# Kernel tuning notes

Hardware: AMD Instinct MI355X
Metric: run time of the kernel (lower is better)

The kernel has to match this reference:

```python
import jax, jax.numpy as jnp
import numpy as np


def setup_inputs() -> dict:
    key = jax.random.key(0)
    k1, k2 = jax.random.split(key)
    B, C, H, W = 8, 128, 48, 48
    x = jax.random.normal(k1, (B, C, H, W), dtype=jnp.float32)
    y = jax.random.normal(k2, (B, C, H, W), dtype=jnp.float32)
    return {"x": x, "y": y}


def reference(x, y):
    # Pairwise squared-distance cost volume.
    # Original computes full Gram matrices xx, yy only for their diagonals;
    # here we compute the squared norms directly (same math, O(N*C) instead of O(N^2*C)).
    B, C, H, W = x.shape
    N = H * W
    xf = x.reshape(B, C, N)  # [B, C, N]
    yf = y.reshape(B, C, N)
    sx = jnp.sum(xf * xf, axis=1)  # [B, N], ||x_i||^2 (diag of x^T x)
    sy = jnp.sum(yf * yf, axis=1)  # [B, N], ||y_j||^2 (diag of y^T y)
    zz = jnp.einsum('bci,bcj->bij', yf, xf)  # zz[b,i,j] = y_i . x_j
    # P[b,i,j] = ||x_i||^2 + ||y_j||^2 - 2 * y_i . x_j  (matches rx^T + ry - 2*zz)
    P = sx[:, :, None] + sy[:, None, :] - 2.0 * zz
    return P.reshape(B, W * H, H, W)
```

## Files before the change

### kernel.cpp

```cpp
#include <hip/hip_runtime.h>

#define NTOK 2304
#define CC   128

typedef __attribute__((ext_vector_type(8))) short bf16x8;
typedef __attribute__((ext_vector_type(4))) float f32x4;

__device__ __forceinline__ unsigned f2bf(float f) {
  unsigned u = __builtin_bit_cast(unsigned, f);
  u += 0x7FFFu + ((u >> 16) & 1u);
  return (u >> 16) & 0xFFFFu;
}
__device__ __forceinline__ unsigned pk2(float a, float b) {
  return f2bf(a) | (f2bf(b) << 16);
}

__device__ __forceinline__ void g2l16(const void* g, void* l) {
  __builtin_amdgcn_global_load_lds(
      (const __attribute__((address_space(1))) unsigned int*)g,
      (__attribute__((address_space(3))) unsigned int*)l, 16, 0, 0);
}

__global__ __launch_bounds__(256) void pwd_prep(
    const float* __restrict__ x, const float* __restrict__ y,
    char* __restrict__ imgX, char* __restrict__ imgY,
    float* __restrict__ sx, float* __restrict__ sy) {
  __shared__ float part[8][32];
  const int tid = threadIdx.x;
  const int nl  = tid & 31;
  const int cg  = tid >> 5;
  const int n   = blockIdx.x * 32 + nl;
  const int b   = blockIdx.y;
  const int sel = blockIdx.z;
  const float* src = sel ? y : x;
  char* img = sel ? imgY : imgX;

  const float* p = src + ((size_t)b * CC + cg * 16) * NTOK + n;
  float v[16];
#pragma unroll
  for (int k = 0; k < 16; ++k) v[k] = p[(size_t)k * NTOK];

  float s = 0.f;
#pragma unroll
  for (int k = 0; k < 16; ++k) s = fmaf(v[k], v[k], s);
  part[cg][nl] = s;

  char* row = img + ((size_t)b * NTOK + n) * 256;
  const int swz = (n & 15) ^ ((n >> 4) & 3);
#pragma unroll
  for (int oo = 0; oo < 2; ++oo) {
    const int o = cg * 2 + oo;
    uint4 wv;
    wv.x = pk2(v[oo * 8 + 0], v[oo * 8 + 1]);
    wv.y = pk2(v[oo * 8 + 2], v[oo * 8 + 3]);
    wv.z = pk2(v[oo * 8 + 4], v[oo * 8 + 5]);
    wv.w = pk2(v[oo * 8 + 6], v[oo * 8 + 7]);
    *(uint4*)(row + ((o ^ swz) * 16)) = wv;
  }
  __syncthreads();
  if (tid < 32) {
    float t = 0.f;
#pragma unroll
    for (int g = 0; g < 8; ++g) t += part[g][tid];
    (sel ? sy : sx)[b * NTOK + blockIdx.x * 32 + tid] = t;
  }
}

__global__ __launch_bounds__(256, 5) void pwd_gemm(
    const char* __restrict__ imgX, const char* __restrict__ imgY,
    const float* __restrict__ sx, const float* __restrict__ sy,
    float* __restrict__ out) {
  __shared__ __attribute__((aligned(16))) char smem[32768];
  char* const smX = smem;
  char* const smY = smem + 16384;

  const int tid = threadIdx.x;

  const int bid = blockIdx.x;
  const int b   = bid & 7;
  const int rem = bid >> 3;
  const int byy = rem / 36;
  const int bxx = rem - byy * 36;
  const int i0 = byy * 64;
  const int j0 = bxx * 64;

  const int w  = tid >> 6;
  const int l  = tid & 63;
  const int lr = l & 15;
  const int lg = l >> 4;
  const int wi = w * 16;

  {
    const char* gx = imgX + ((size_t)b * NTOK + j0) * 256;
    const char* gy = imgY + ((size_t)b * NTOK + i0) * 256;
    const int wb = w * 4096;
    const size_t o0 = (size_t)wb + (size_t)l * 16;
#pragma unroll
    for (int it = 0; it < 4; ++it)
      g2l16(gx + o0 + it * 1024, smX + wb + it * 1024);
#pragma unroll
    for (int it = 0; it < 4; ++it)
      g2l16(gy + o0 + it * 1024, smY + wb + it * 1024);
  }

  const float sxr = sx[b * NTOK + i0 + wi + lr];
  f32x4 syq[4];
#pragma unroll
  for (int mf = 0; mf < 4; ++mf)
    syq[mf] = *(const f32x4*)(sy + b * NTOK + j0 + mf * 16 + lg * 4);

  __syncthreads();

  f32x4 acc[4] = {};
#pragma unroll
  for (int ks = 0; ks < 4; ++ks) {
    const int o = ks * 4 + lg;
    bf16x8 ax[4], by;
#pragma unroll
    for (int mf = 0; mf < 4; ++mf) {
      const int n = mf * 16 + lr;
      const int slot = o ^ (n & 15) ^ ((n >> 4) & 3);
      ax[mf] = *(const bf16x8*)(smX + n * 256 + slot * 16);
    }
    {
      const int n = wi + lr;
      const int slot = o ^ (n & 15) ^ ((n >> 4) & 3);
      by = *(const bf16x8*)(smY + n * 256 + slot * 16);
    }
#pragma unroll
    for (int mf = 0; mf < 4; ++mf)
      acc[mf] = __builtin_amdgcn_mfma_f32_16x16x32_bf16(ax[mf], by, acc[mf],
                                                        0, 0, 0);
  }

  {
    float* const tile = (float*)smem;
    __syncthreads();
#pragma unroll
    for (int mf = 0; mf < 4; ++mf) {
      f32x4 vv;
#pragma unroll
      for (int r = 0; r < 4; ++r)
        vv[r] = sxr + syq[mf][r] - 2.0f * acc[mf][r];
      const int row = wi + lr;
      const int c16 = mf * 4 + lg;
      *(f32x4*)((char*)tile + row * 256 + ((c16 ^ (row & 15)) * 16)) = vv;
    }
    __syncthreads();
#pragma unroll
    for (int it = 0; it < 4; ++it) {
      const int c   = it * 256 + tid;
      const int row = c >> 4;
      const int c16 = c & 15;
      f32x4 vv = *(const f32x4*)((char*)tile + row * 256 +
                                 ((c16 ^ (row & 15)) * 16));
      __builtin_nontemporal_store(
          vv, (f32x4*)(out + ((size_t)b * NTOK + i0 + row) * NTOK + j0 + c16 * 4));
    }
  }
}

extern "C" void kernel_launch(void* const* d_in, const int* in_sizes, int n_in,
                              void* d_out, int out_size, void* d_ws, size_t ws_size,
                              hipStream_t stream) {
  (void)in_sizes; (void)n_in; (void)out_size; (void)ws_size;
  const float* x = (const float*)d_in[0];
  const float* y = (const float*)d_in[1];
  float* out = (float*)d_out;

  char* imgX = (char*)d_ws;
  char* imgY = imgX + (size_t)8 * NTOK * 256;
  float* sx  = (float*)(imgY + (size_t)8 * NTOK * 256);
  float* sy  = sx + 8 * NTOK;

  dim3 gp(NTOK / 32, 8, 2);
  pwd_prep<<<gp, dim3(256), 0, stream>>>(x, y, imgX, imgY, sx, sy);

  dim3 gg(36 * 36 * 8);
  pwd_gemm<<<gg, dim3(256), 0, stream>>>(imgX, imgY, sx, sy, out);
}
```

Baseline: 42.89 us.

## Process two 64-column X tiles per block, prefetching the second into registers

```diff
diff --git a/kernel.cpp b/kernel.cpp
--- a/kernel.cpp
+++ b/kernel.cpp
@@ -79,10 +79,10 @@
   const int bid = blockIdx.x;
   const int b   = bid & 7;
   const int rem = bid >> 3;
-  const int byy = rem / 36;
-  const int bxx = rem - byy * 36;
+  const int byy = rem / 18;
+  const int bxx = rem - byy * 18;
   const int i0 = byy * 64;
-  const int j0 = bxx * 64;
+  const int j0 = bxx * 128;
 
   const int w  = tid >> 6;
   const int l  = tid & 63;
@@ -90,9 +90,10 @@
   const int lg = l >> 4;
   const int wi = w * 16;
 
+  const char* gx = imgX + ((size_t)b * NTOK + j0) * 256;
+  const char* gy = imgY + ((size_t)b * NTOK + i0) * 256;
+
   {
-    const char* gx = imgX + ((size_t)b * NTOK + j0) * 256;
-    const char* gy = imgY + ((size_t)b * NTOK + i0) * 256;
     const int wb = w * 4096;
     const size_t o0 = (size_t)wb + (size_t)l * 16;
 #pragma unroll
@@ -102,12 +103,16 @@
     for (int it = 0; it < 4; ++it)
       g2l16(gy + o0 + it * 1024, smY + wb + it * 1024);
   }
+  uint4 breg[4];
+#pragma unroll
+  for (int it = 0; it < 4; ++it)
+    breg[it] = *(const uint4*)(gx + 16384 + tid * 16 + it * 4096);
 
   const float sxr = sx[b * NTOK + i0 + wi + lr];
-  f32x4 syq[4];
+  f32x4 syqA[4];
 #pragma unroll
   for (int mf = 0; mf < 4; ++mf)
-    syq[mf] = *(const f32x4*)(sy + b * NTOK + j0 + mf * 16 + lg * 4);
+    syqA[mf] = *(const f32x4*)(sy + b * NTOK + j0 + mf * 16 + lg * 4);
 
   __syncthreads();
 
@@ -133,30 +138,85 @@
                                                         0, 0, 0);
   }
 
-  {
-    float* const tile = (float*)smem;
-    __syncthreads();
+  float* const tile = (float*)smX;
+  __syncthreads();
+#pragma unroll
+  for (int mf = 0; mf < 4; ++mf) {
+    f32x4 vv;
+#pragma unroll
+    for (int r = 0; r < 4; ++r)
+      vv[r] = sxr + syqA[mf][r] - 2.0f * acc[mf][r];
+    const int row = wi + lr;
+    const int c16 = mf * 4 + lg;
+    *(f32x4*)((char*)tile + row * 256 + ((c16 ^ (row & 15)) * 16)) = vv;
+  }
+  __syncthreads();
+#pragma unroll
+  for (int it = 0; it < 4; ++it) {
+    const int c   = it * 256 + tid;
+    const int row = c >> 4;
+    const int c16 = c & 15;
+    f32x4 vv = *(const f32x4*)((char*)tile + row * 256 +
+                               ((c16 ^ (row & 15)) * 16));
+    __builtin_nontemporal_store(
+        vv, (f32x4*)(out + ((size_t)b * NTOK + i0 + row) * NTOK + j0 + c16 * 4));
+  }
+
+  f32x4 syqB[4];
+#pragma unroll
+  for (int mf = 0; mf < 4; ++mf)
+    syqB[mf] = *(const f32x4*)(sy + b * NTOK + j0 + 64 + mf * 16 + lg * 4);
+
+  __syncthreads();
+
+#pragma unroll
+  for (int it = 0; it < 4; ++it)
+    *(uint4*)(smX + tid * 16 + it * 4096) = breg[it];
+  __syncthreads();
+
+  f32x4 acc2[4] = {};
+#pragma unroll
+  for (int ks = 0; ks < 4; ++ks) {
+    const int o = ks * 4 + lg;
+    bf16x8 ax[4], by;
 #pragma unroll
     for (int mf = 0; mf < 4; ++mf) {
-      f32x4 vv;
-#pragma unroll
-      for (int r = 0; r < 4; ++r)
-        vv[r] = sxr + syq[mf][r] - 2.0f * acc[mf][r];
-      const int row = wi + lr;
-      const int c16 = mf * 4 + lg;
-      *(f32x4*)((char*)tile + row * 256 + ((c16 ^ (row & 15)) * 16)) = vv;
-    }
-    __syncthreads();
-#pragma unroll
-    for (int it = 0; it < 4; ++it) {
-      const int c   = it * 256 + tid;
-      const int row = c >> 4;
-      const int c16 = c & 15;
-      f32x4 vv = *(const f32x4*)((char*)tile + row * 256 +
-                                 ((c16 ^ (row & 15)) * 16));
-      __builtin_nontemporal_store(
-          vv, (f32x4*)(out + ((size_t)b * NTOK + i0 + row) * NTOK + j0 + c16 * 4));
-    }
+      const int n = mf * 16 + lr;
+      const int slot = o ^ (n & 15) ^ ((n >> 4) & 3);
+      ax[mf] = *(const bf16x8*)(smX + n * 256 + slot * 16);
+    }
+    {
+      const int n = wi + lr;
+      const int slot = o ^ (n & 15) ^ ((n >> 4) & 3);
+      by = *(const bf16x8*)(smY + n * 256 + slot * 16);
+    }
+#pragma unroll
+    for (int mf = 0; mf < 4; ++mf)
+      acc2[mf] = __builtin_amdgcn_mfma_f32_16x16x32_bf16(ax[mf], by, acc2[mf],
+                                                         0, 0, 0);
+  }
+
+  __syncthreads();
+#pragma unroll
+  for (int mf = 0; mf < 4; ++mf) {
+    f32x4 vv;
+#pragma unroll
+    for (int r = 0; r < 4; ++r)
+      vv[r] = sxr + syqB[mf][r] - 2.0f * acc2[mf][r];
+    const int row = wi + lr;
+    const int c16 = mf * 4 + lg;
+    *(f32x4*)((char*)tile + row * 256 + ((c16 ^ (row & 15)) * 16)) = vv;
+  }
+  __syncthreads();
+#pragma unroll
+  for (int it = 0; it < 4; ++it) {
+    const int c   = it * 256 + tid;
+    const int row = c >> 4;
+    const int c16 = c & 15;
+    f32x4 vv = *(const f32x4*)((char*)tile + row * 256 +
+                               ((c16 ^ (row & 15)) * 16));
+    __builtin_nontemporal_store(
+        vv, (f32x4*)(out + ((size_t)b * NTOK + i0 + row) * NTOK + j0 + 64 + c16 * 4));
   }
 }
 
@@ -176,6 +236,6 @@
   dim3 gp(NTOK / 32, 8, 2);
   pwd_prep<<<gp, dim3(256), 0, stream>>>(x, y, imgX, imgY, sx, sy);
 
-  dim3 gg(36 * 36 * 8);
+  dim3 gg(36 * 18 * 8);
   pwd_gemm<<<gg, dim3(256), 0, stream>>>(imgX, imgY, sx, sy, out);
 }
```

New measurement: 55.91 us. +30.4%, slower.

## Pre-pack MFMA fragment layout and load operands directly from global memory

Applied to the files above, without the earlier changes.

```diff
diff --git a/kernel.cpp b/kernel.cpp
--- a/kernel.cpp
+++ b/kernel.cpp
@@ -2,6 +2,7 @@
 
 #define NTOK 2304
 #define CC   128
+#define IMB  ((size_t)NTOK * 256)
 
 typedef __attribute__((ext_vector_type(8))) short bf16x8;
 typedef __attribute__((ext_vector_type(4))) float f32x4;
@@ -13,12 +14,6 @@
 }
 __device__ __forceinline__ unsigned pk2(float a, float b) {
   return f2bf(a) | (f2bf(b) << 16);
-}
-
-__device__ __forceinline__ void g2l16(const void* g, void* l) {
-  __builtin_amdgcn_global_load_lds(
-      (const __attribute__((address_space(1))) unsigned int*)g,
-      (__attribute__((address_space(3))) unsigned int*)l, 16, 0, 0);
 }
 
 __global__ __launch_bounds__(256) void pwd_prep(
@@ -33,7 +28,7 @@
   const int b   = blockIdx.y;
   const int sel = blockIdx.z;
   const float* src = sel ? y : x;
-  char* img = sel ? imgY : imgX;
+  char* img = (sel ? imgY : imgX) + (size_t)b * IMB;
 
   const float* p = src + ((size_t)b * CC + cg * 16) * NTOK + n;
   float v[16];
@@ -45,8 +40,7 @@
   for (int k = 0; k < 16; ++k) s = fmaf(v[k], v[k], s);
   part[cg][nl] = s;
 
-  char* row = img + ((size_t)b * NTOK + n) * 256;
-  const int swz = (n & 15) ^ ((n >> 4) & 3);
+  const int rbase = (n >> 4) * 4096 + (n & 15) * 16;
 #pragma unroll
   for (int oo = 0; oo < 2; ++oo) {
     const int o = cg * 2 + oo;
@@ -55,7 +49,7 @@
     wv.y = pk2(v[oo * 8 + 2], v[oo * 8 + 3]);
     wv.z = pk2(v[oo * 8 + 4], v[oo * 8 + 5]);
     wv.w = pk2(v[oo * 8 + 6], v[oo * 8 + 7]);
-    *(uint4*)(row + ((o ^ swz) * 16)) = wv;
+    *(uint4*)(img + rbase + (o >> 2) * 1024 + (o & 3) * 256) = wv;
   }
   __syncthreads();
   if (tid < 32) {
@@ -66,96 +60,75 @@
   }
 }
 
-__global__ __launch_bounds__(256, 5) void pwd_gemm(
+__global__ __launch_bounds__(256, 4) void pwd_gemm(
     const char* __restrict__ imgX, const char* __restrict__ imgY,
     const float* __restrict__ sx, const float* __restrict__ sy,
     float* __restrict__ out) {
-  __shared__ __attribute__((aligned(16))) char smem[32768];
-  char* const smX = smem;
-  char* const smY = smem + 16384;
+  __shared__ __attribute__((aligned(16))) char smem[16384];
 
   const int tid = threadIdx.x;
+  const int w  = tid >> 6;
+  const int l  = tid & 63;
+  const int lr = l & 15;
+  const int lg = l >> 4;
 
   const int bid = blockIdx.x;
   const int b   = bid & 7;
   const int rem = bid >> 3;
-  const int byy = rem / 36;
-  const int bxx = rem - byy * 36;
+  const int byy = rem / 9;
+  const int bxq = rem - byy * 9;
   const int i0 = byy * 64;
-  const int j0 = bxx * 64;
+  const int j0 = bxq * 256 + w * 64;
 
-  const int w  = tid >> 6;
-  const int l  = tid & 63;
-  const int lr = l & 15;
-  const int lg = l >> 4;
-  const int wi = w * 16;
+  const char* gA = imgX + (size_t)b * IMB + (j0 >> 4) * 4096;
+  const char* gB = imgY + (size_t)b * IMB + (i0 >> 4) * 4096;
 
-  {
-    const char* gx = imgX + ((size_t)b * NTOK + j0) * 256;
-    const char* gy = imgY + ((size_t)b * NTOK + i0) * 256;
-    const int wb = w * 4096;
-    const size_t o0 = (size_t)wb + (size_t)l * 16;
+  f32x4 acc[4][4] = {};
 #pragma unroll
-    for (int it = 0; it < 4; ++it)
-      g2l16(gx + o0 + it * 1024, smX + wb + it * 1024);
+  for (int ks = 0; ks < 4; ++ks) {
+    bf16x8 a[4], bv[4];
 #pragma unroll
-    for (int it = 0; it < 4; ++it)
-      g2l16(gy + o0 + it * 1024, smY + wb + it * 1024);
+    for (int mf = 0; mf < 4; ++mf)
+      a[mf] = *(const bf16x8*)(gA + mf * 4096 + ks * 1024 + l * 16);
+#pragma unroll
+    for (int nf = 0; nf < 4; ++nf)
+      bv[nf] = *(const bf16x8*)(gB + nf * 4096 + ks * 1024 + l * 16);
+#pragma unroll
+    for (int mf = 0; mf < 4; ++mf)
+#pragma unroll
+      for (int nf = 0; nf < 4; ++nf)
+        acc[mf][nf] = __builtin_amdgcn_mfma_f32_16x16x32_bf16(
+            a[mf], bv[nf], acc[mf][nf], 0, 0, 0);
   }
 
-  const float sxr = sx[b * NTOK + i0 + wi + lr];
+  float sxr[4];
+#pragma unroll
+  for (int nf = 0; nf < 4; ++nf)
+    sxr[nf] = sx[b * NTOK + i0 + nf * 16 + lr];
   f32x4 syq[4];
 #pragma unroll
   for (int mf = 0; mf < 4; ++mf)
     syq[mf] = *(const f32x4*)(sy + b * NTOK + j0 + mf * 16 + lg * 4);
 
-  __syncthreads();
-
-  f32x4 acc[4] = {};
+  char* const myb = smem + w * 4096;
 #pragma unroll
-  for (int ks = 0; ks < 4; ++ks) {
-    const int o = ks * 4 + lg;
-    bf16x8 ax[4], by;
-#pragma unroll
-    for (int mf = 0; mf < 4; ++mf) {
-      const int n = mf * 16 + lr;
-      const int slot = o ^ (n & 15) ^ ((n >> 4) & 3);
-      ax[mf] = *(const bf16x8*)(smX + n * 256 + slot * 16);
-    }
-    {
-      const int n = wi + lr;
-      const int slot = o ^ (n & 15) ^ ((n >> 4) & 3);
-      by = *(const bf16x8*)(smY + n * 256 + slot * 16);
-    }
-#pragma unroll
-    for (int mf = 0; mf < 4; ++mf)
-      acc[mf] = __builtin_amdgcn_mfma_f32_16x16x32_bf16(ax[mf], by, acc[mf],
-                                                        0, 0, 0);
-  }
-
-  {
-    float* const tile = (float*)smem;
-    __syncthreads();
+  for (int nf = 0; nf < 4; ++nf) {
 #pragma unroll
     for (int mf = 0; mf < 4; ++mf) {
       f32x4 vv;
 #pragma unroll
       for (int r = 0; r < 4; ++r)
-        vv[r] = sxr + syq[mf][r] - 2.0f * acc[mf][r];
-      const int row = wi + lr;
+        vv[r] = sxr[nf] + syq[mf][r] - 2.0f * acc[mf][nf][r];
       const int c16 = mf * 4 + lg;
-      *(f32x4*)((char*)tile + row * 256 + ((c16 ^ (row & 15)) * 16)) = vv;
+      *(f32x4*)(myb + lr * 256 + ((c16 ^ lr) * 16)) = vv;
     }
-    __syncthreads();
 #pragma unroll
     for (int it = 0; it < 4; ++it) {
-      const int c   = it * 256 + tid;
-      const int row = c >> 4;
-      const int c16 = c & 15;
-      f32x4 vv = *(const f32x4*)((char*)tile + row * 256 +
-                                 ((c16 ^ (row & 15)) * 16));
+      const int row = it * 4 + lg;
+      f32x4 vv = *(const f32x4*)(myb + row * 256 + ((lr ^ row) * 16));
       __builtin_nontemporal_store(
-          vv, (f32x4*)(out + ((size_t)b * NTOK + i0 + row) * NTOK + j0 + c16 * 4));
+          vv, (f32x4*)(out + ((size_t)b * NTOK + i0 + nf * 16 + row) * NTOK +
+                       j0 + lr * 4));
     }
   }
 }
@@ -169,13 +142,13 @@
   float* out = (float*)d_out;
 
   char* imgX = (char*)d_ws;
-  char* imgY = imgX + (size_t)8 * NTOK * 256;
-  float* sx  = (float*)(imgY + (size_t)8 * NTOK * 256);
+  char* imgY = imgX + 8 * IMB;
+  float* sx  = (float*)(imgY + 8 * IMB);
   float* sy  = sx + 8 * NTOK;
 
   dim3 gp(NTOK / 32, 8, 2);
   pwd_prep<<<gp, dim3(256), 0, stream>>>(x, y, imgX, imgY, sx, sy);
 
-  dim3 gg(36 * 36 * 8);
+  dim3 gg(36 * 9 * 8);
   pwd_gemm<<<gg, dim3(256), 0, stream>>>(imgX, imgY, sx, sy, out);
 }
```

After: 48.57 us. 13.2% more time.
